# Kernel optimization log

Hardware: AMD Instinct MI355X
Metric: run time of the kernel (lower is better)

The kernel has to match this reference:

```python
import jax, jax.numpy as jnp
import numpy as np

B, T, S0 = 8, 4, 4096
D_MODEL, H, D, R, RANK = 2048, 16, 128, 64, 512
C = D - R  # content dim = 64


def _rope(x, positions):
    # x: [B, H, T, R]; rotate-half style RoPE as in the torch module
    half = x.shape[-1] // 2
    inv_freq = 1.0 / (10000.0 ** (jnp.arange(half, dtype=jnp.float32) / half))
    freqs = positions.astype(jnp.float32)[:, None] * inv_freq[None, :]  # [T, half]
    cos = jnp.cos(freqs)[None, None].astype(x.dtype)
    sin = jnp.sin(freqs)[None, None].astype(x.dtype)
    x1, x2 = x[..., :half], x[..., half:]
    return jnp.concatenate([x1 * cos - x2 * sin, x1 * sin + x2 * cos], axis=-1)


def setup_inputs() -> dict:
    key = jax.random.key(0)
    ks = jax.random.split(key, 9)
    s = 0.02
    return {
        "x": jax.random.normal(ks[0], (B, T, D_MODEL), jnp.float32),
        "cache_c_kv": jax.random.normal(ks[1], (B, S0, RANK), jnp.float32),
        "cache_k_rope": jax.random.normal(ks[2], (B, S0, H, R), jnp.float32),
        "w_q": jax.random.normal(ks[3], (D_MODEL, H * C), jnp.float32) * s,
        "w_q_rope": jax.random.normal(ks[4], (D_MODEL, H * R), jnp.float32) * s,
        "w_kv_down": jax.random.normal(ks[5], (D_MODEL, RANK), jnp.float32) * s,
        "w_kv_up": jax.random.normal(ks[6], (RANK, H * D), jnp.float32) * s,
        "w_k_rope": jax.random.normal(ks[7], (D_MODEL, H * R), jnp.float32) * s,
        "w_out": jax.random.normal(ks[8], (H * D, D_MODEL), jnp.float32) * s,
    }


def reference(x, cache_c_kv, cache_k_rope, w_q, w_q_rope, w_kv_down, w_kv_up, w_k_rope, w_out):
    cache_len = cache_c_kv.shape[1]
    positions = jnp.arange(cache_len, cache_len + T)

    # queries
    q_content = (x @ w_q).reshape(B, T, H, C).transpose(0, 2, 1, 3)        # [B,H,T,C]
    q_rope = (x @ w_q_rope).reshape(B, T, H, R).transpose(0, 2, 1, 3)      # [B,H,T,R]
    q_rope = _rope(q_rope, positions)
    q = jnp.concatenate([q_content, q_rope], axis=-1)                       # [B,H,T,D]

    # new compressed kv + rope keys, append to cache
    c_kv_new = x @ w_kv_down                                                # [B,T,RANK]
    k_rope_new = (x @ w_k_rope).reshape(B, T, H, R).transpose(0, 2, 1, 3)
    k_rope_new = _rope(k_rope_new, positions).transpose(0, 2, 1, 3)         # [B,T,H,R]
    c_kv = jnp.concatenate([cache_c_kv, c_kv_new], axis=1)                  # [B,S,RANK]
    k_rope = jnp.concatenate([cache_k_rope, k_rope_new], axis=1)            # [B,S,H,R]

    # decompress full cache every step (the expensive MLA pattern)
    S = c_kv.shape[1]
    kv = (c_kv @ w_kv_up).reshape(B, S, H, D)                               # [B,S,H,D]
    k_content = kv[..., :C].transpose(0, 2, 1, 3)                           # [B,H,S,C]
    v = kv.transpose(0, 2, 1, 3)                                            # [B,H,S,D]
    k = jnp.concatenate([k_content, k_rope.transpose(0, 2, 1, 3)], axis=-1) # [B,H,S,D]

    # kv_cache present => is_prefill False => no causal mask (faithful to source)
    scale = 1.0 / jnp.sqrt(jnp.asarray(D, dtype=q.dtype))
    scores = jnp.einsum('bhtd,bhsd->bhts', q, k) * scale
    attn = jax.nn.softmax(scores, axis=-1)
    out = jnp.einsum('bhts,bhsd->bhtd', attn, v)                            # [B,H,T,D]
    out = out.transpose(0, 2, 1, 3).reshape(B, T, H * D)
    return out @ w_out                                                       # [B,T,D_MODEL]
```

## Files before the change

kernel.cpp:

```cpp
#include <hip/hip_runtime.h>
#include <hip/hip_fp16.h>
#include <cmath>

#define BB 8
#define TT 4
#define HH 16
#define DDIM 128
#define RRDIM 64
#define CCDIM 64
#define RANKC 512
#define DMODEL 2048
#define S0C 4096
#define NQ 64
#define HD 2048
#define NACT 3584
#define NSC 65
#define NG 17
#define SPAD 4160
#define SCALE_ATT 0.08838834764831845f

typedef __attribute__((ext_vector_type(8))) short bf16x8;
typedef __attribute__((ext_vector_type(4))) float f32x4;
typedef unsigned short ushortT;

#define AIDX(row, kk) ((row)*132 + (((row)>>2)<<2) + (kk))

static __device__ __forceinline__ unsigned short f2bf(float x) {
  unsigned u = __float_as_uint(x);
  u += 0x7FFFu + ((u >> 16) & 1u);
  return (unsigned short)(u >> 16);
}
static __device__ __forceinline__ unsigned pk2(float a, float b) {
  return (unsigned)f2bf(a) | ((unsigned)f2bf(b) << 16);
}

__global__ __launch_bounds__(256) void k_front(const float* __restrict__ A,
                                               const float* __restrict__ w0,
                                               const float* __restrict__ w1,
                                               const float* __restrict__ w2,
                                               const float* __restrict__ w3,
                                               const float* __restrict__ cckv,
                                               float* __restrict__ part,
                                               ushortT* __restrict__ ckvB,
                                               ushortT* __restrict__ ckvT,
                                               float* __restrict__ rctab) {
  __shared__ float shf[4352];
  const int tid = threadIdx.x;
  const int bx = blockIdx.x;
  if (bx < 448) {
    const int cb = bx % 28;
    const int k0 = (bx / 28) * 128;
    const float* W; int N, lc0, off;
    if (cb < 8)       { W = w0; N = 1024; lc0 = cb * 128;        off = 0; }
    else if (cb < 16) { W = w1; N = 1024; lc0 = (cb - 8) * 128;  off = 1024; }
    else if (cb < 20) { W = w2; N = 512;  lc0 = (cb - 16) * 128; off = 2048; }
    else              { W = w3; N = 1024; lc0 = (cb - 20) * 128; off = 2560; }
    {
      const int row = tid >> 3;
      const int kseg = (tid & 7) * 16;
      const float4* s4 = reinterpret_cast<const float4*>(A + (size_t)row * DMODEL + k0 + kseg);
      float4 v0 = s4[0], v1 = s4[1], v2 = s4[2], v3 = s4[3];
      *reinterpret_cast<float4*>(&shf[AIDX(row, kseg)])      = v0;
      *reinterpret_cast<float4*>(&shf[AIDX(row, kseg + 4)])  = v1;
      *reinterpret_cast<float4*>(&shf[AIDX(row, kseg + 8)])  = v2;
      *reinterpret_cast<float4*>(&shf[AIDX(row, kseg + 12)]) = v3;
    }
    __syncthreads();
    const int cg = tid & 31;
    const int rg = tid >> 5;
    float acc[4][4];
    #pragma unroll
    for (int r = 0; r < 4; ++r)
      #pragma unroll
      for (int c = 0; c < 4; ++c) acc[r][c] = 0.f;
    #pragma unroll 4
    for (int kk = 0; kk < 128; ++kk) {
      const float4 w4 = *reinterpret_cast<const float4*>(W + (size_t)(k0 + kk) * N + lc0 + cg * 4);
      const float wv[4] = {w4.x, w4.y, w4.z, w4.w};
      #pragma unroll
      for (int r = 0; r < 4; ++r) {
        const float av = shf[AIDX(rg * 4 + r, kk)];
        #pragma unroll
        for (int c = 0; c < 4; ++c) acc[r][c] = fmaf(av, wv[c], acc[r][c]);
      }
    }
    #pragma unroll
    for (int r = 0; r < 4; ++r) {
      float4 o = make_float4(acc[r][0], acc[r][1], acc[r][2], acc[r][3]);
      *reinterpret_cast<float4*>(part + ((size_t)(bx / 28) * 32 + rg * 4 + r) * NACT + off + lc0 + cg * 4) = o;
    }
  } else if (bx < 960) {
    ushortT* tlds = reinterpret_cast<ushortT*>(shf);
    const int idx = bx - 448;
    const int b = idx >> 6, c = idx & 63;
    const float* src = cckv + ((size_t)b * S0C + c * 64) * RANKC;
    ushortT* dstB = ckvB + ((size_t)(b * NSC + c) * 64) * RANKC;
    ushortT* dstT = ckvT + ((size_t)(b * NSC + c) * RANKC) * 64;
    const int s = tid >> 2, rq = tid & 3;
    const int rloc = tid >> 1, shalf = (tid & 1) * 32;
    for (int slab = 0; slab < 4; ++slab) {
      const int r0 = slab * 128;
      unsigned pk_arr[16];
      #pragma unroll
      for (int i = 0; i < 8; ++i) {
        const float4 v = *reinterpret_cast<const float4*>(src + (size_t)s * RANKC + r0 + rq * 32 + i * 4);
        pk_arr[2 * i]     = pk2(v.x, v.y);
        pk_arr[2 * i + 1] = pk2(v.z, v.w);
        *reinterpret_cast<uint2*>(&tlds[s * 136 + rq * 32 + i * 4]) =
            make_uint2(pk_arr[2 * i], pk_arr[2 * i + 1]);
      }
      {
        uint4* db = reinterpret_cast<uint4*>(dstB + (size_t)s * RANKC + r0 + rq * 32);
        db[0] = make_uint4(pk_arr[0], pk_arr[1], pk_arr[2], pk_arr[3]);
        db[1] = make_uint4(pk_arr[4], pk_arr[5], pk_arr[6], pk_arr[7]);
        db[2] = make_uint4(pk_arr[8], pk_arr[9], pk_arr[10], pk_arr[11]);
        db[3] = make_uint4(pk_arr[12], pk_arr[13], pk_arr[14], pk_arr[15]);
      }
      __syncthreads();
      unsigned pkv[16];
      #pragma unroll
      for (int k = 0; k < 16; ++k) {
        const unsigned t0 = tlds[(shalf + 2 * k)     * 136 + rloc];
        const unsigned t1 = tlds[(shalf + 2 * k + 1) * 136 + rloc];
        pkv[k] = t0 | (t1 << 16);
      }
      uint4* d = reinterpret_cast<uint4*>(dstT + ((size_t)(r0 + rloc)) * 64 + shalf);
      d[0] = make_uint4(pkv[0], pkv[1], pkv[2], pkv[3]);
      d[1] = make_uint4(pkv[4], pkv[5], pkv[6], pkv[7]);
      d[2] = make_uint4(pkv[8], pkv[9], pkv[10], pkv[11]);
      d[3] = make_uint4(pkv[12], pkv[13], pkv[14], pkv[15]);
      __syncthreads();
    }
  } else {
    const int b = bx - 960;
    const uint4 z = make_uint4(0, 0, 0, 0);
    uint4* p = reinterpret_cast<uint4*>(ckvT + ((size_t)(b * NSC + 64) * RANKC) * 64);
    for (int i = tid; i < 4096; i += 256) p[i] = z;
    uint4* q = reinterpret_cast<uint4*>(ckvB + (((size_t)(b * NSC + 64) * 64) + 4) * RANKC);
    for (int i = tid; i < 3840; i += 256) q[i] = z;
    if (bx == 960 && tid < 128) {
      const int t = tid >> 5, j = tid & 31;
      const double fr = (double)(S0C + t) * pow(10000.0, -(double)j / 32.0);
      rctab[t * 32 + j]       = (float)cos(fr);
      rctab[128 + t * 32 + j] = (float)sin(fr);
    }
  }
}

__global__ __launch_bounds__(256) void k_mid(const float* __restrict__ part0,
                                             const float* __restrict__ cache_kr,
                                             const float* __restrict__ wup,
                                             const float* __restrict__ rctab,
                                             ushortT* __restrict__ qlat,
                                             ushortT* __restrict__ ckvB,
                                             ushortT* __restrict__ ckvT,
                                             __half* __restrict__ rs) {
  __shared__ float smid[2176];
  const int tid = threadIdx.x;
  const int bx = blockIdx.x;
  if (bx < 1152) {
    const int bh = bx / 9, sy = bx % 9;
    const int b = bh >> 4, h = bh & 15;
    float* raw_q = smid;
    float* raw_k = smid + 256;
    float* qr_l  = smid + 512;
    float* kr_l  = smid + 768;
    {
      const int t = tid >> 6, j = tid & 63;
      const size_t rowoff = (size_t)(b * TT + t) * NACT;
      float sq = 0.f, sk = 0.f;
      #pragma unroll 4
      for (int ks = 0; ks < 16; ++ks) {
        const float* pp = part0 + (size_t)ks * (32 * NACT) + rowoff;
        sq += pp[1024 + h * 64 + j];
        sk += pp[2560 + h * 64 + j];
      }
      raw_q[t * 64 + j] = sq;
      raw_k[t * 64 + j] = sk;
    }
    __syncthreads();
    {
      const int t = tid >> 6, j = tid & 63;
      const int j2 = j & 31;
      const float cs = rctab[t * 32 + j2];
      const float sn = rctab[128 + t * 32 + j2];
      const float qa = raw_q[t * 64 + j], qp = raw_q[t * 64 + (j ^ 32)];
      const float ka = raw_k[t * 64 + j], kp = raw_k[t * 64 + (j ^ 32)];
      float qv, kv;
      if (j < 32) { qv = qa * cs - qp * sn; kv = ka * cs - kp * sn; }
      else        { qv = qp * sn + qa * cs; kv = kp * sn + ka * cs; }
      qr_l[t * 64 + j] = qv * SCALE_ATT;
      kr_l[t * 64 + j] = kv;
    }
    __syncthreads();
    const int ql = tid & 3;
    float4 qf[4][4];
    #pragma unroll
    for (int t = 0; t < 4; ++t)
      #pragma unroll
      for (int u = 0; u < 4; ++u)
        qf[t][u] = *reinterpret_cast<const float4*>(&qr_l[t * 64 + ql * 16 + u * 4]);
    const int s0 = sy * 512;
    #pragma unroll 2
    for (int pass = 0; pass < 8; ++pass) {
      const int s = s0 + pass * 64 + (tid >> 2);
      if (s < 4100) {
        float p[4] = {0.f, 0.f, 0.f, 0.f};
        const float* krow = (s < S0C)
            ? cache_kr + (((size_t)b * S0C + s) * HH + h) * RRDIM
            : &kr_l[(s - S0C) * 64];
        #pragma unroll
        for (int u = 0; u < 4; ++u) {
          const float4 kv = *reinterpret_cast<const float4*>(krow + ql * 16 + u * 4);
          #pragma unroll
          for (int t = 0; t < 4; ++t)
            p[t] += kv.x * qf[t][u].x + kv.y * qf[t][u].y
                  + kv.z * qf[t][u].z + kv.w * qf[t][u].w;
        }
        #pragma unroll
        for (int t = 0; t < 4; ++t) {
          p[t] += __shfl_xor(p[t], 1, 4);
          p[t] += __shfl_xor(p[t], 2, 4);
        }
        rs[((size_t)bh * 4 + ql) * SPAD + s] = __float2half(p[ql]);
      }
    }
  } else if (bx < 1216) {
    const int lx = bx - 1152;
    const int h = lx & 15;
    const int r0 = (lx >> 4) * 128;
    float* a_s = smid;
    {
      const int bt = tid >> 3;
      const int c8 = (tid & 7) * 8;
      float v[8] = {0.f,0.f,0.f,0.f,0.f,0.f,0.f,0.f};
      #pragma unroll 4
      for (int ks = 0; ks < 16; ++ks) {
        const float4* pp = reinterpret_cast<const float4*>(
            part0 + (size_t)ks * (32 * NACT) + (size_t)bt * NACT + h * CCDIM + c8);
        const float4 x0 = pp[0], x1 = pp[1];
        v[0]+=x0.x; v[1]+=x0.y; v[2]+=x0.z; v[3]+=x0.w;
        v[4]+=x1.x; v[5]+=x1.y; v[6]+=x1.z; v[7]+=x1.w;
      }
      #pragma unroll
      for (int u = 0; u < 8; ++u) a_s[bt * 68 + c8 + u] = v[u];
    }
    __syncthreads();
    const int r = tid & 127;
    const int bth = tid >> 7;
    const float* wrow = wup + (size_t)(r0 + r) * HD + h * DDIM;
    float4 wreg[16];
    #pragma unroll
    for (int u = 0; u < 16; ++u)
      wreg[u] = *reinterpret_cast<const float4*>(wrow + u * 4);
    float acc[16];
    #pragma unroll
    for (int i = 0; i < 16; ++i) acc[i] = 0.f;
    #pragma unroll
    for (int u = 0; u < 16; ++u) {
      #pragma unroll
      for (int i = 0; i < 16; ++i) {
        const float4 av = *reinterpret_cast<const float4*>(&a_s[(bth * 16 + i) * 68 + u * 4]);
        acc[i] = fmaf(av.x, wreg[u].x, acc[i]);
        acc[i] = fmaf(av.y, wreg[u].y, acc[i]);
        acc[i] = fmaf(av.z, wreg[u].z, acc[i]);
        acc[i] = fmaf(av.w, wreg[u].w, acc[i]);
      }
    }
    #pragma unroll
    for (int i = 0; i < 16; ++i) {
      const int bt = bth * 16 + i;
      const int b = bt >> 2, t = bt & 3;
      qlat[((size_t)(b * NQ) + h * TT + t) * RANKC + r0 + r] = f2bf(acc[i]);
    }
  } else {
    const int g = (bx - 1216) * 256 + tid;
    const int r = g & 511;
    const int bt = g >> 9;
    const int b = bt >> 2, t = bt & 3;
    float s = 0.f;
    #pragma unroll 4
    for (int ks = 0; ks < 16; ++ks)
      s += part0[(size_t)ks * (32 * NACT) + (size_t)bt * NACT + 2048 + r];
    const ushortT bv = f2bf(s);
    ckvB[(((size_t)(b * NSC + 64) * 64) + t) * RANKC + r] = bv;
    ckvT[(((size_t)(b * NSC + 64) * RANKC) + r) * 64 + t] = bv;
  }
}

__global__ __launch_bounds__(256) void k_att(
    const ushortT* __restrict__ ckvB, const ushortT* __restrict__ ckvT,
    const ushortT* __restrict__ qlat, const __half* __restrict__ rs,
    float* __restrict__ olat, float* __restrict__ mlg) {
  __shared__ ushortT PL[4][32 * 72];
  __shared__ float mlS[4][2][32];
  __shared__ float wS[4][32];
  const int tid = threadIdx.x;
  const int wv = tid >> 6;
  const int lane = tid & 63;
  const int lm = lane & 15, lg = lane >> 4;
  const int g = blockIdx.x, b = blockIdx.y, qh = blockIdx.z;
  const int qbase = qh * 32;
  const int nc = (g < 16) ? 4 : 1;
  const int c0 = (g < 16) ? g * 4 : 64;

  if (wv < nc) {
    const int myc = c0 + wv;
    const int scnt = (myc < 64) ? 64 : TT;
    const ushortT* bsrc = ckvB + ((size_t)(b * NSC + myc) * 64) * RANKC;
    const ushortT* qrow = qlat + ((size_t)b * NQ + qbase + lm) * RANKC + lg * 8;
    f32x4 acc[2][4];
    #pragma unroll
    for (int qm = 0; qm < 2; ++qm)
      #pragma unroll
      for (int st = 0; st < 4; ++st) acc[qm][st] = (f32x4){0.f, 0.f, 0.f, 0.f};
    #pragma unroll
    for (int ks = 0; ks < 16; ++ks) {
      const bf16x8 qa0 = *reinterpret_cast<const bf16x8*>(qrow + ks * 32);
      const bf16x8 qa1 = *reinterpret_cast<const bf16x8*>(qrow + 16 * RANKC + ks * 32);
      #pragma unroll
      for (int st = 0; st < 4; ++st) {
        const bf16x8 bf = *reinterpret_cast<const bf16x8*>(
            bsrc + (size_t)(st * 16 + lm) * RANKC + ks * 32 + lg * 8);
        acc[0][st] = __builtin_amdgcn_mfma_f32_16x16x32_bf16(qa0, bf, acc[0][st], 0, 0, 0);
        acc[1][st] = __builtin_amdgcn_mfma_f32_16x16x32_bf16(qa1, bf, acc[1][st], 0, 0, 0);
      }
    }
    #pragma unroll
    for (int qm = 0; qm < 2; ++qm) {
      #pragma unroll
      for (int reg = 0; reg < 4; ++reg) {
        const int ql = qm * 16 + lg * 4 + reg;
        const int qi = qbase + ql;
        const __half* rp = rs + (((size_t)(b * HH) + (qi >> 2)) * TT + (qi & 3)) * SPAD + myc * 64;
        float vvv[4];
        float mx = -1e30f;
        #pragma unroll
        for (int st = 0; st < 4; ++st) {
          const int sl = st * 16 + lm;
          const float val = (sl < scnt)
              ? fmaf(acc[qm][st][reg], SCALE_ATT, __half2float(rp[sl]))
              : -1e30f;
          vvv[st] = val;
          mx = fmaxf(mx, val);
        }
        #pragma unroll
        for (int off = 1; off < 16; off <<= 1) mx = fmaxf(mx, __shfl_xor(mx, off, 16));
        float sum = 0.f;
        #pragma unroll
        for (int st = 0; st < 4; ++st) {
          const float p = __expf(vvv[st] - mx);
          vvv[st] = p;
          sum += p;
        }
        #pragma unroll
        for (int off = 1; off < 16; off <<= 1) sum += __shfl_xor(sum, off, 16);
        #pragma unroll
        for (int st = 0; st < 4; ++st)
          PL[wv][ql * 72 + st * 16 + lm] = f2bf(vvv[st]);
        if (lm == 0) { mlS[wv][0][ql] = mx; mlS[wv][1][ql] = sum; }
      }
    }
  }
  __syncthreads();

  if (tid < 32) {
    const int q = tid;
    float mg = -1e30f;
    for (int c = 0; c < nc; ++c) mg = fmaxf(mg, mlS[c][0][q]);
    float la = 0.f;
    for (int c = 0; c < nc; ++c) {
      const float w = __expf(mlS[c][0][q] - mg);
      wS[c][q] = w;
      la = fmaf(mlS[c][1][q], w, la);
    }
    const size_t gb = (((size_t)b * NG + g) * NQ + qbase + q) * 2;
    mlg[gb] = mg; mlg[gb + 1] = la;
  }
  __syncthreads();

  const int rg = wv;
  f32x4 OACC[2][8];
  #pragma unroll
  for (int qm = 0; qm < 2; ++qm)
    #pragma unroll
    for (int rn = 0; rn < 8; ++rn) OACC[qm][rn] = (f32x4){0.f, 0.f, 0.f, 0.f};
  for (int c = 0; c < nc; ++c) {
    const bf16x8 pa00 = *reinterpret_cast<const bf16x8*>(&PL[c][lm * 72 + lg * 8]);
    const bf16x8 pa01 = *reinterpret_cast<const bf16x8*>(&PL[c][lm * 72 + 32 + lg * 8]);
    const bf16x8 pa10 = *reinterpret_cast<const bf16x8*>(&PL[c][(16 + lm) * 72 + lg * 8]);
    const bf16x8 pa11 = *reinterpret_cast<const bf16x8*>(&PL[c][(16 + lm) * 72 + 32 + lg * 8]);
    const f32x4 w0 = {wS[c][lg * 4 + 0], wS[c][lg * 4 + 1], wS[c][lg * 4 + 2], wS[c][lg * 4 + 3]};
    const f32x4 w1 = {wS[c][16 + lg * 4 + 0], wS[c][16 + lg * 4 + 1],
                      wS[c][16 + lg * 4 + 2], wS[c][16 + lg * 4 + 3]};
    const ushortT* vb = ckvT + ((size_t)(b * NSC + c0 + c) * RANKC + rg * 128 + lm) * 64 + lg * 8;
    #pragma unroll
    for (int rn = 0; rn < 8; ++rn) {
      const bf16x8 b0 = *reinterpret_cast<const bf16x8*>(vb + (size_t)rn * 16 * 64);
      const bf16x8 b1 = *reinterpret_cast<const bf16x8*>(vb + (size_t)rn * 16 * 64 + 32);
      f32x4 t0 = (f32x4){0.f, 0.f, 0.f, 0.f}, t1 = (f32x4){0.f, 0.f, 0.f, 0.f};
      t0 = __builtin_amdgcn_mfma_f32_16x16x32_bf16(pa00, b0, t0, 0, 0, 0);
      t0 = __builtin_amdgcn_mfma_f32_16x16x32_bf16(pa01, b1, t0, 0, 0, 0);
      t1 = __builtin_amdgcn_mfma_f32_16x16x32_bf16(pa10, b0, t1, 0, 0, 0);
      t1 = __builtin_amdgcn_mfma_f32_16x16x32_bf16(pa11, b1, t1, 0, 0, 0);
      OACC[0][rn] += w0 * t0;
      OACC[1][rn] += w1 * t1;
    }
  }
  const size_t obase = ((size_t)(b * NG + g) * NQ) * RANKC;
  #pragma unroll
  for (int qm = 0; qm < 2; ++qm)
    #pragma unroll
    for (int rn = 0; rn < 8; ++rn)
      #pragma unroll
      for (int reg = 0; reg < 4; ++reg)
        olat[obase + (size_t)(qbase + qm * 16 + lg * 4 + reg) * RANKC + rg * 128 + rn * 16 + lm]
            = OACC[qm][rn][reg];
}

__global__ __launch_bounds__(512) void k_combF(const float* __restrict__ mlg,
                                               const float* __restrict__ olat,
                                               const float* __restrict__ wup,
                                               float* __restrict__ ohead,
                                               float* __restrict__ out) {
  __shared__ float wrow[4][20];
  __shared__ float att_lds[4][516];
  __shared__ float red[4][4][32][4];
  const int h = blockIdx.x, b = blockIdx.y;
  const int tid = threadIdx.x;
  {
    const int t = tid >> 7, col = tid & 127;
    out[(size_t)(b * TT + t) * HD + h * DDIM + col] = 0.f;
  }
  const int wave = tid >> 6;
  const int i = wave >> 1;
  const int rhalf = wave & 1;
  const int rl = tid & 63;
  const int qi = h * TT + i;
  float m1 = -1e30f, l1 = 0.f;
  if (rl < NG) {
    const size_t base = (((size_t)b * NG + rl) * NQ + qi) * 2;
    m1 = mlg[base]; l1 = mlg[base + 1];
  }
  float M = m1;
  #pragma unroll
  for (int off = 1; off < 64; off <<= 1) M = fmaxf(M, __shfl_xor(M, off));
  float L = (rl < NG) ? l1 * __expf(m1 - M) : 0.f;
  #pragma unroll
  for (int off = 1; off < 64; off <<= 1) L += __shfl_xor(L, off);
  const float invL = 1.0f / L;
  if (rl < NG) wrow[i][rl] = __expf(m1 - M) * invL;
  __syncthreads();
  const int r0 = rhalf * 256 + rl * 4;
  {
    float o0 = 0.f, o1 = 0.f, o2 = 0.f, o3 = 0.f;
    for (int c = 0; c < NG; ++c) {
      const float w = wrow[i][c];
      const float4 v = *reinterpret_cast<const float4*>(
          olat + (((size_t)b * NG + c) * NQ + qi) * RANKC + r0);
      o0 = fmaf(v.x, w, o0); o1 = fmaf(v.y, w, o1);
      o2 = fmaf(v.z, w, o2); o3 = fmaf(v.w, w, o3);
    }
    *reinterpret_cast<float4*>(&att_lds[i][r0]) = make_float4(o0, o1, o2, o3);
  }
  __syncthreads();
  const int t = tid >> 7;
  const int rq = (tid >> 5) & 3;
  const int c4 = tid & 31;
  const float* wb = wup + (size_t)h * DDIM + c4 * 4;
  float a0 = 0.f, a1 = 0.f, a2 = 0.f, a3 = 0.f;
  const int rbeg = rq * 128;
  #pragma unroll 4
  for (int rr = 0; rr < 128; ++rr) {
    const int r = rbeg + rr;
    const float4 w4 = *reinterpret_cast<const float4*>(wb + (size_t)r * HD);
    const float a = att_lds[t][r];
    a0 = fmaf(a, w4.x, a0); a1 = fmaf(a, w4.y, a1);
    a2 = fmaf(a, w4.z, a2); a3 = fmaf(a, w4.w, a3);
  }
  *reinterpret_cast<float4*>(&red[rq][t][c4][0]) = make_float4(a0, a1, a2, a3);
  __syncthreads();
  if (tid < 128) {
    const int t2 = tid >> 5, c42 = tid & 31;
    float4 s = make_float4(0.f, 0.f, 0.f, 0.f);
    #pragma unroll
    for (int q = 0; q < 4; ++q) {
      const float4 v = *reinterpret_cast<const float4*>(&red[q][t2][c42][0]);
      s.x += v.x; s.y += v.y; s.z += v.z; s.w += v.w;
    }
    *reinterpret_cast<float4*>(&ohead[(size_t)(b * TT + t2) * HD + h * DDIM + c42 * 4]) = s;
  }
}

__global__ __launch_bounds__(256) void k_projA(const float* __restrict__ A,
                                               const float* __restrict__ W,
                                               float* __restrict__ out) {
  __shared__ float a_lds[4352];
  const int tid = threadIdx.x;
  const int c0 = blockIdx.x * 128;
  const int k0 = blockIdx.y * 128;
  {
    const int row = tid >> 3;
    const int kseg = (tid & 7) * 16;
    const float4* s4 = reinterpret_cast<const float4*>(A + (size_t)row * DMODEL + k0 + kseg);
    float4 v0 = s4[0], v1 = s4[1], v2 = s4[2], v3 = s4[3];
    *reinterpret_cast<float4*>(&a_lds[AIDX(row, kseg)])      = v0;
    *reinterpret_cast<float4*>(&a_lds[AIDX(row, kseg + 4)])  = v1;
    *reinterpret_cast<float4*>(&a_lds[AIDX(row, kseg + 8)])  = v2;
    *reinterpret_cast<float4*>(&a_lds[AIDX(row, kseg + 12)]) = v3;
  }
  __syncthreads();
  const int cg = tid & 31;
  const int rg = tid >> 5;
  float acc[4][4];
  #pragma unroll
  for (int r = 0; r < 4; ++r)
    #pragma unroll
    for (int c = 0; c < 4; ++c) acc[r][c] = 0.f;
  #pragma unroll 4
  for (int kk = 0; kk < 128; ++kk) {
    const float4 w4 = *reinterpret_cast<const float4*>(W + (size_t)(k0 + kk) * HD + c0 + cg * 4);
    const float wv[4] = {w4.x, w4.y, w4.z, w4.w};
    #pragma unroll
    for (int r = 0; r < 4; ++r) {
      const float av = a_lds[AIDX(rg * 4 + r, kk)];
      #pragma unroll
      for (int c = 0; c < 4; ++c) acc[r][c] = fmaf(av, wv[c], acc[r][c]);
    }
  }
  #pragma unroll
  for (int r = 0; r < 4; ++r)
    #pragma unroll
    for (int c = 0; c < 4; ++c)
      unsafeAtomicAdd(&out[(size_t)(rg * 4 + r) * HD + c0 + cg * 4 + c], acc[r][c]);
}

extern "C" void kernel_launch(void* const* d_in, const int* in_sizes, int n_in,
                              void* d_out, int out_size, void* d_ws, size_t ws_size,
                              hipStream_t stream) {
  const float* x     = (const float*)d_in[0];
  const float* cckv  = (const float*)d_in[1];
  const float* ckr   = (const float*)d_in[2];
  const float* w_q   = (const float*)d_in[3];
  const float* w_qr  = (const float*)d_in[4];
  const float* w_kvd = (const float*)d_in[5];
  const float* w_kvu = (const float*)d_in[6];
  const float* w_kr  = (const float*)d_in[7];
  const float* w_out = (const float*)d_in[8];
  float* out = (float*)d_out;
  float* ws = (float*)d_ws;

  size_t off = 0;
  ushortT* qlat   = (ushortT*)(ws + off); off += 131072;
  float* mlgb     = ws + off; off += (size_t)BB * NG * NQ * 2;
  float* ohead    = ws + off; off += 65536;
  float* rctab    = ws + off; off += 256;
  __half* rsb     = (__half*)(ws + off); off += 1064960;
  ushortT* ckvB   = (ushortT*)(ws + off); off += 8519680;
  ushortT* ckvT   = (ushortT*)(ws + off); off += 8519680;
  float* regB  = ws + off;
  float* part0 = regB;
  float* olat  = regB;

  k_front<<<dim3(968), 256, 0, stream>>>(x, w_q, w_qr, w_kvd, w_kr, cckv, part0, ckvB, ckvT, rctab);
  k_mid<<<dim3(1280), 256, 0, stream>>>(part0, ckr, w_kvu, rctab, qlat, ckvB, ckvT, rsb);
  k_att<<<dim3(NG, BB, 2), 256, 0, stream>>>(ckvB, ckvT, qlat, rsb, olat, mlgb);
  k_combF<<<dim3(16, 8), 512, 0, stream>>>(mlgb, olat, w_kvu, ohead, out);
  k_projA<<<dim3(16, 16), 256, 0, stream>>>(ohead, w_out, out);
}
```

Measured before the change: 194.6 us.

## Split combine/projection over rank quarters, prefetch rope keys, raise MFMA priority

k_combF is split across four rank quarters in a new grid dimension. Each block writes a partial head output, and k_projA sums these partials while loading its A tile, using a K-split of 64 over twice as many blocks. The rope-score loop in k_mid now double-buffers the cache key loads, and the tail rows get their own path. s_setprio is raised around the MFMA loops in k_att. The aim is more parallelism in the small tail kernels and hiding memory latency, at the cost of extra partial-buffer traffic and more atomics in k_projA.

```diff
diff --git a/kernel.cpp b/kernel.cpp
--- a/kernel.cpp
+++ b/kernel.cpp
@@ -137,7 +137,7 @@
     uint4* p = reinterpret_cast<uint4*>(ckvT + ((size_t)(b * NSC + 64) * RANKC) * 64);
     for (int i = tid; i < 4096; i += 256) p[i] = z;
     uint4* q = reinterpret_cast<uint4*>(ckvB + (((size_t)(b * NSC + 64) * 64) + 4) * RANKC);
-    for (int i = tid; i < 3840; i += 256) q[i] = z;
+    for (int i = tid; i < 3840; i += 256) p = p, q[i] = z;
     if (bx == 960 && tid < 128) {
       const int t = tid >> 5, j = tid & 31;
       const double fr = (double)(S0C + t) * pow(10000.0, -(double)j / 32.0);
@@ -200,15 +200,42 @@
       #pragma unroll
       for (int u = 0; u < 4; ++u)
         qf[t][u] = *reinterpret_cast<const float4*>(&qr_l[t * 64 + ql * 16 + u * 4]);
-    const int s0 = sy * 512;
-    #pragma unroll 2
-    for (int pass = 0; pass < 8; ++pass) {
-      const int s = s0 + pass * 64 + (tid >> 2);
-      if (s < 4100) {
+    if (sy < 8) {
+      const int s0 = sy * 512;
+      const int sloc = tid >> 2;
+      const float* base = cache_kr + (((size_t)b * S0C + s0 + sloc) * HH + h) * RRDIM + ql * 16;
+      const size_t sstep = (size_t)64 * HH * RRDIM;
+      float4 bA[4], bB[4];
+      #pragma unroll
+      for (int u = 0; u < 4; ++u) bA[u] = *reinterpret_cast<const float4*>(base + u * 4);
+      #pragma unroll
+      for (int pass = 0; pass < 8; ++pass) {
+        float4* cur = (pass & 1) ? bB : bA;
+        float4* nxt = (pass & 1) ? bA : bB;
+        if (pass < 7) {
+          const float* nb = base + (size_t)(pass + 1) * sstep;
+          #pragma unroll
+          for (int u = 0; u < 4; ++u) nxt[u] = *reinterpret_cast<const float4*>(nb + u * 4);
+        }
         float p[4] = {0.f, 0.f, 0.f, 0.f};
-        const float* krow = (s < S0C)
-            ? cache_kr + (((size_t)b * S0C + s) * HH + h) * RRDIM
-            : &kr_l[(s - S0C) * 64];
+        #pragma unroll
+        for (int u = 0; u < 4; ++u)
+          #pragma unroll
+          for (int t = 0; t < 4; ++t)
+            p[t] += cur[u].x * qf[t][u].x + cur[u].y * qf[t][u].y
+                  + cur[u].z * qf[t][u].z + cur[u].w * qf[t][u].w;
+        #pragma unroll
+        for (int t = 0; t < 4; ++t) {
+          p[t] += __shfl_xor(p[t], 1, 4);
+          p[t] += __shfl_xor(p[t], 2, 4);
+        }
+        rs[((size_t)bh * 4 + ql) * SPAD + s0 + pass * 64 + sloc] = __float2half(p[ql]);
+      }
+    } else {
+      const int sloc = tid >> 2;
+      if (sloc < TT) {
+        const float* krow = &kr_l[sloc * 64];
+        float p[4] = {0.f, 0.f, 0.f, 0.f};
         #pragma unroll
         for (int u = 0; u < 4; ++u) {
           const float4 kv = *reinterpret_cast<const float4*>(krow + ql * 16 + u * 4);
@@ -222,7 +249,7 @@
           p[t] += __shfl_xor(p[t], 1, 4);
           p[t] += __shfl_xor(p[t], 2, 4);
         }
-        rs[((size_t)bh * 4 + ql) * SPAD + s] = __float2half(p[ql]);
+        rs[((size_t)bh * 4 + ql) * SPAD + S0C + sloc] = __float2half(p[ql]);
       }
     }
   } else if (bx < 1216) {
@@ -314,6 +341,7 @@
     for (int qm = 0; qm < 2; ++qm)
       #pragma unroll
       for (int st = 0; st < 4; ++st) acc[qm][st] = (f32x4){0.f, 0.f, 0.f, 0.f};
+    __builtin_amdgcn_s_setprio(1);
     #pragma unroll
     for (int ks = 0; ks < 16; ++ks) {
       const bf16x8 qa0 = *reinterpret_cast<const bf16x8*>(qrow + ks * 32);
@@ -326,6 +354,7 @@
         acc[1][st] = __builtin_amdgcn_mfma_f32_16x16x32_bf16(qa1, bf, acc[1][st], 0, 0, 0);
       }
     }
+    __builtin_amdgcn_s_setprio(0);
     #pragma unroll
     for (int qm = 0; qm < 2; ++qm) {
       #pragma unroll
@@ -394,6 +423,7 @@
     const f32x4 w1 = {wS[c][16 + lg * 4 + 0], wS[c][16 + lg * 4 + 1],
                       wS[c][16 + lg * 4 + 2], wS[c][16 + lg * 4 + 3]};
     const ushortT* vb = ckvT + ((size_t)(b * NSC + c0 + c) * RANKC + rg * 128 + lm) * 64 + lg * 8;
+    __builtin_amdgcn_s_setprio(1);
     #pragma unroll
     for (int rn = 0; rn < 8; ++rn) {
       const bf16x8 b0 = *reinterpret_cast<const bf16x8*>(vb + (size_t)rn * 16 * 64);
@@ -406,6 +436,7 @@
       OACC[0][rn] += w0 * t0;
       OACC[1][rn] += w1 * t1;
     }
+    __builtin_amdgcn_s_setprio(0);
   }
   const size_t obase = ((size_t)(b * NG + g) * NQ) * RANKC;
   #pragma unroll
@@ -418,23 +449,22 @@
             = OACC[qm][rn][reg];
 }
 
-__global__ __launch_bounds__(512) void k_combF(const float* __restrict__ mlg,
+__global__ __launch_bounds__(256) void k_combF(const float* __restrict__ mlg,
                                                const float* __restrict__ olat,
                                                const float* __restrict__ wup,
-                                               float* __restrict__ ohead,
+                                               float* __restrict__ oheadP,
                                                float* __restrict__ out) {
   __shared__ float wrow[4][20];
-  __shared__ float att_lds[4][516];
-  __shared__ float red[4][4][32][4];
-  const int h = blockIdx.x, b = blockIdx.y;
+  __shared__ float red[2][4][32][4];
+  __shared__ float att_l[4][128];
+  const int h = blockIdx.x, b = blockIdx.y, rq = blockIdx.z;
   const int tid = threadIdx.x;
-  {
-    const int t = tid >> 7, col = tid & 127;
-    out[(size_t)(b * TT + t) * HD + h * DDIM + col] = 0.f;
-  }
-  const int wave = tid >> 6;
-  const int i = wave >> 1;
-  const int rhalf = wave & 1;
+  if (rq == 0) {
+    const int t = tid >> 6, col2 = (tid & 63) * 2;
+    out[(size_t)(b * TT + t) * HD + h * DDIM + col2] = 0.f;
+    out[(size_t)(b * TT + t) * HD + h * DDIM + col2 + 1] = 0.f;
+  }
+  const int i = tid >> 6;
   const int rl = tid & 63;
   const int qi = h * TT + i;
   float m1 = -1e30f, l1 = 0.f;
@@ -451,63 +481,80 @@
   const float invL = 1.0f / L;
   if (rl < NG) wrow[i][rl] = __expf(m1 - M) * invL;
   __syncthreads();
-  const int r0 = rhalf * 256 + rl * 4;
   {
+    const int ch = tid >> 7;
+    const int t = (tid >> 5) & 3;
+    const int p32 = tid & 31;
+    const int qit = h * TT + t;
+    const int cbeg = ch ? 9 : 0, cend = ch ? NG : 9;
     float o0 = 0.f, o1 = 0.f, o2 = 0.f, o3 = 0.f;
-    for (int c = 0; c < NG; ++c) {
-      const float w = wrow[i][c];
+    #pragma unroll 3
+    for (int c = cbeg; c < cend; ++c) {
+      const float w = wrow[t][c];
       const float4 v = *reinterpret_cast<const float4*>(
-          olat + (((size_t)b * NG + c) * NQ + qi) * RANKC + r0);
+          olat + (((size_t)b * NG + c) * NQ + qit) * RANKC + rq * 128 + p32 * 4);
       o0 = fmaf(v.x, w, o0); o1 = fmaf(v.y, w, o1);
       o2 = fmaf(v.z, w, o2); o3 = fmaf(v.w, w, o3);
     }
-    *reinterpret_cast<float4*>(&att_lds[i][r0]) = make_float4(o0, o1, o2, o3);
-  }
-  __syncthreads();
-  const int t = tid >> 7;
-  const int rq = (tid >> 5) & 3;
-  const int c4 = tid & 31;
-  const float* wb = wup + (size_t)h * DDIM + c4 * 4;
-  float a0 = 0.f, a1 = 0.f, a2 = 0.f, a3 = 0.f;
-  const int rbeg = rq * 128;
-  #pragma unroll 4
-  for (int rr = 0; rr < 128; ++rr) {
-    const int r = rbeg + rr;
-    const float4 w4 = *reinterpret_cast<const float4*>(wb + (size_t)r * HD);
-    const float a = att_lds[t][r];
-    a0 = fmaf(a, w4.x, a0); a1 = fmaf(a, w4.y, a1);
-    a2 = fmaf(a, w4.z, a2); a3 = fmaf(a, w4.w, a3);
-  }
-  *reinterpret_cast<float4*>(&red[rq][t][c4][0]) = make_float4(a0, a1, a2, a3);
+    *reinterpret_cast<float4*>(&red[ch][t][p32][0]) = make_float4(o0, o1, o2, o3);
+  }
   __syncthreads();
   if (tid < 128) {
-    const int t2 = tid >> 5, c42 = tid & 31;
-    float4 s = make_float4(0.f, 0.f, 0.f, 0.f);
-    #pragma unroll
-    for (int q = 0; q < 4; ++q) {
-      const float4 v = *reinterpret_cast<const float4*>(&red[q][t2][c42][0]);
-      s.x += v.x; s.y += v.y; s.z += v.z; s.w += v.w;
-    }
-    *reinterpret_cast<float4*>(&ohead[(size_t)(b * TT + t2) * HD + h * DDIM + c42 * 4]) = s;
-  }
-}
-
-__global__ __launch_bounds__(256) void k_projA(const float* __restrict__ A,
+    const int t = tid >> 5, p32 = tid & 31;
+    const float4 v0 = *reinterpret_cast<const float4*>(&red[0][t][p32][0]);
+    const float4 v1 = *reinterpret_cast<const float4*>(&red[1][t][p32][0]);
+    *reinterpret_cast<float4*>(&att_l[t][p32 * 4]) =
+        make_float4(v0.x + v1.x, v0.y + v1.y, v0.z + v1.z, v0.w + v1.w);
+  }
+  __syncthreads();
+  {
+    const int rhalf = tid >> 7;
+    const int t = (tid >> 5) & 3;
+    const int c4 = tid & 31;
+    const float* wb = wup + (size_t)(rq * 128 + rhalf * 64) * HD + h * DDIM + c4 * 4;
+    float a0 = 0.f, a1 = 0.f, a2 = 0.f, a3 = 0.f;
+    #pragma unroll 4
+    for (int rr = 0; rr < 64; ++rr) {
+      const float4 w4 = *reinterpret_cast<const float4*>(wb + (size_t)rr * HD);
+      const float a = att_l[t][rhalf * 64 + rr];
+      a0 = fmaf(a, w4.x, a0); a1 = fmaf(a, w4.y, a1);
+      a2 = fmaf(a, w4.z, a2); a3 = fmaf(a, w4.w, a3);
+    }
+    *reinterpret_cast<float4*>(&red[rhalf][t][c4][0]) = make_float4(a0, a1, a2, a3);
+  }
+  __syncthreads();
+  if (tid < 128) {
+    const int t = tid >> 5, c4 = tid & 31;
+    const float4 v0 = *reinterpret_cast<const float4*>(&red[0][t][c4][0]);
+    const float4 v1 = *reinterpret_cast<const float4*>(&red[1][t][c4][0]);
+    *reinterpret_cast<float4*>(
+        &oheadP[(((size_t)rq * 32) + b * TT + t) * HD + h * DDIM + c4 * 4]) =
+        make_float4(v0.x + v1.x, v0.y + v1.y, v0.z + v1.z, v0.w + v1.w);
+  }
+}
+
+__global__ __launch_bounds__(256) void k_projA(const float* __restrict__ oheadP,
                                                const float* __restrict__ W,
                                                float* __restrict__ out) {
-  __shared__ float a_lds[4352];
+  __shared__ float a_lds[2176];
   const int tid = threadIdx.x;
   const int c0 = blockIdx.x * 128;
-  const int k0 = blockIdx.y * 128;
+  const int k0 = blockIdx.y * 64;
   {
     const int row = tid >> 3;
-    const int kseg = (tid & 7) * 16;
-    const float4* s4 = reinterpret_cast<const float4*>(A + (size_t)row * DMODEL + k0 + kseg);
-    float4 v0 = s4[0], v1 = s4[1], v2 = s4[2], v3 = s4[3];
-    *reinterpret_cast<float4*>(&a_lds[AIDX(row, kseg)])      = v0;
-    *reinterpret_cast<float4*>(&a_lds[AIDX(row, kseg + 4)])  = v1;
-    *reinterpret_cast<float4*>(&a_lds[AIDX(row, kseg + 8)])  = v2;
-    *reinterpret_cast<float4*>(&a_lds[AIDX(row, kseg + 12)]) = v3;
+    const int kseg = (tid & 7) * 8;
+    float4 s0 = make_float4(0.f, 0.f, 0.f, 0.f), s1 = s0;
+    #pragma unroll
+    for (int p = 0; p < 4; ++p) {
+      const float4* v4 = reinterpret_cast<const float4*>(
+          oheadP + ((size_t)p * 32 + row) * HD + k0 + kseg);
+      const float4 a = v4[0], bq = v4[1];
+      s0.x += a.x;  s0.y += a.y;  s0.z += a.z;  s0.w += a.w;
+      s1.x += bq.x; s1.y += bq.y; s1.z += bq.z; s1.w += bq.w;
+    }
+    const int base = row * 68 + kseg;
+    *reinterpret_cast<float4*>(&a_lds[base]) = s0;
+    *reinterpret_cast<float4*>(&a_lds[base + 4]) = s1;
   }
   __syncthreads();
   const int cg = tid & 31;
@@ -518,12 +565,12 @@
     #pragma unroll
     for (int c = 0; c < 4; ++c) acc[r][c] = 0.f;
   #pragma unroll 4
-  for (int kk = 0; kk < 128; ++kk) {
+  for (int kk = 0; kk < 64; ++kk) {
     const float4 w4 = *reinterpret_cast<const float4*>(W + (size_t)(k0 + kk) * HD + c0 + cg * 4);
     const float wv[4] = {w4.x, w4.y, w4.z, w4.w};
     #pragma unroll
     for (int r = 0; r < 4; ++r) {
-      const float av = a_lds[AIDX(rg * 4 + r, kk)];
+      const float av = a_lds[(rg * 4 + r) * 68 + kk];
       #pragma unroll
       for (int c = 0; c < 4; ++c) acc[r][c] = fmaf(av, wv[c], acc[r][c]);
     }
@@ -553,7 +600,7 @@
   size_t off = 0;
   ushortT* qlat   = (ushortT*)(ws + off); off += 131072;
   float* mlgb     = ws + off; off += (size_t)BB * NG * NQ * 2;
-  float* ohead    = ws + off; off += 65536;
+  float* oheadP   = ws + off; off += 262144;
   float* rctab    = ws + off; off += 256;
   __half* rsb     = (__half*)(ws + off); off += 1064960;
   ushortT* ckvB   = (ushortT*)(ws + off); off += 8519680;
@@ -565,6 +612,6 @@
   k_front<<<dim3(968), 256, 0, stream>>>(x, w_q, w_qr, w_kvd, w_kr, cckv, part0, ckvB, ckvT, rctab);
   k_mid<<<dim3(1280), 256, 0, stream>>>(part0, ckr, w_kvu, rctab, qlat, ckvB, ckvT, rsb);
   k_att<<<dim3(NG, BB, 2), 256, 0, stream>>>(ckvB, ckvT, qlat, rsb, olat, mlgb);
-  k_combF<<<dim3(16, 8), 512, 0, stream>>>(mlgb, olat, w_kvu, ohead, out);
-  k_projA<<<dim3(16, 16), 256, 0, stream>>>(ohead, w_out, out);
-}
+  k_combF<<<dim3(16, 8, 4), 256, 0, stream>>>(mlgb, olat, w_kvu, oheadP, out);
+  k_projA<<<dim3(16, 32), 256, 0, stream>>>(oheadP, w_out, out);
+}
```

Measured after the change: 197.9 us. Within noise of the previous version (+1.7%).

## Restructure rope-score blocks to read contiguous k_rope rows across all heads

Applied to the files above, without the earlier changes.

The rope-score part of k_mid now gives each block a batch and a 32-position slice covering all 16 heads, so every cache_k_rope row (16 heads × 64) is read contiguously instead of one head-strided 256-byte slice per block. Each of these blocks reduces and ropes the queries for all heads into a 16 KB shared buffer. Eight separate tail blocks compute the scores against the 4 new rope keys. The split partials for q are therefore reduced redundantly by 128 blocks per batch, and shared memory use grows to 32 KB per block, which may lower occupancy.

```diff
diff --git a/kernel.cpp b/kernel.cpp
--- a/kernel.cpp
+++ b/kernel.cpp
@@ -155,78 +155,123 @@
                                              ushortT* __restrict__ ckvB,
                                              ushortT* __restrict__ ckvT,
                                              __half* __restrict__ rs) {
-  __shared__ float smid[2176];
+  __shared__ float smid[8192];
   const int tid = threadIdx.x;
   const int bx = blockIdx.x;
-  if (bx < 1152) {
-    const int bh = bx / 9, sy = bx % 9;
-    const int b = bh >> 4, h = bh & 15;
-    float* raw_q = smid;
-    float* raw_k = smid + 256;
-    float* qr_l  = smid + 512;
-    float* kr_l  = smid + 768;
+  if (bx < 1032) {
+    const bool tail = (bx >= 1024);
+    const int b = tail ? (bx - 1024) : (bx >> 7);
+    float* qS = smid;
     {
-      const int t = tid >> 6, j = tid & 63;
-      const size_t rowoff = (size_t)(b * TT + t) * NACT;
-      float sq = 0.f, sk = 0.f;
-      #pragma unroll 4
-      for (int ks = 0; ks < 16; ++ks) {
-        const float* pp = part0 + (size_t)ks * (32 * NACT) + rowoff;
-        sq += pp[1024 + h * 64 + j];
-        sk += pp[2560 + h * 64 + j];
-      }
-      raw_q[t * 64 + j] = sq;
-      raw_k[t * 64 + j] = sk;
+      float v[16];
+      #pragma unroll
+      for (int r = 0; r < 16; ++r) {
+        const int idx = r * 256 + tid;
+        const int h = idx >> 8, tt = (idx >> 6) & 3, j = idx & 63;
+        float s = 0.f;
+        #pragma unroll 4
+        for (int ks = 0; ks < 16; ++ks)
+          s += part0[(size_t)ks * (32 * NACT) + (size_t)(b * TT + tt) * NACT + 1024 + h * 64 + j];
+        v[r] = s;
+      }
+      #pragma unroll
+      for (int r = 0; r < 16; ++r) qS[r * 256 + tid] = v[r];
     }
     __syncthreads();
     {
-      const int t = tid >> 6, j = tid & 63;
-      const int j2 = j & 31;
-      const float cs = rctab[t * 32 + j2];
-      const float sn = rctab[128 + t * 32 + j2];
-      const float qa = raw_q[t * 64 + j], qp = raw_q[t * 64 + (j ^ 32)];
-      const float ka = raw_k[t * 64 + j], kp = raw_k[t * 64 + (j ^ 32)];
-      float qv, kv;
-      if (j < 32) { qv = qa * cs - qp * sn; kv = ka * cs - kp * sn; }
-      else        { qv = qp * sn + qa * cs; kv = kp * sn + ka * cs; }
-      qr_l[t * 64 + j] = qv * SCALE_ATT;
-      kr_l[t * 64 + j] = kv;
+      float rv[16];
+      #pragma unroll
+      for (int r = 0; r < 16; ++r) {
+        const int idx = r * 256 + tid;
+        const int tt = (idx >> 6) & 3, j = idx & 63, j2 = j & 31;
+        const float cs = rctab[tt * 32 + j2];
+        const float sn = rctab[128 + tt * 32 + j2];
+        const float a = qS[idx], p = qS[idx ^ 32];
+        rv[r] = ((j < 32) ? (a * cs - p * sn) : (p * sn + a * cs)) * SCALE_ATT;
+      }
+      __syncthreads();
+      #pragma unroll
+      for (int r = 0; r < 16; ++r) qS[r * 256 + tid] = rv[r];
     }
     __syncthreads();
-    const int ql = tid & 3;
-    float4 qf[4][4];
-    #pragma unroll
-    for (int t = 0; t < 4; ++t)
-      #pragma unroll
-      for (int u = 0; u < 4; ++u)
-        qf[t][u] = *reinterpret_cast<const float4*>(&qr_l[t * 64 + ql * 16 + u * 4]);
-    const int s0 = sy * 512;
-    #pragma unroll 2
-    for (int pass = 0; pass < 8; ++pass) {
-      const int s = s0 + pass * 64 + (tid >> 2);
-      if (s < 4100) {
-        float p[4] = {0.f, 0.f, 0.f, 0.f};
-        const float* krow = (s < S0C)
-            ? cache_kr + (((size_t)b * S0C + s) * HH + h) * RRDIM
-            : &kr_l[(s - S0C) * 64];
-        #pragma unroll
-        for (int u = 0; u < 4; ++u) {
-          const float4 kv = *reinterpret_cast<const float4*>(krow + ql * 16 + u * 4);
+    if (!tail) {
+      const int s0 = (bx & 127) * 32;
+      const int sloc = tid >> 3;
+      const int j8 = (tid & 7) * 8;
+      const int bh4 = b * HH * 4;
+      const float* krow = cache_kr + ((size_t)(b * S0C + s0 + sloc)) * (HH * RRDIM);
+      #pragma unroll 4
+      for (int h = 0; h < 16; ++h) {
+        const float4 k0 = *reinterpret_cast<const float4*>(krow + h * 64 + j8);
+        const float4 k1 = *reinterpret_cast<const float4*>(krow + h * 64 + j8 + 4);
+        float p[4];
+        #pragma unroll
+        for (int t = 0; t < 4; ++t) {
+          const float4 q0 = *reinterpret_cast<const float4*>(&qS[h * 256 + t * 64 + j8]);
+          const float4 q1 = *reinterpret_cast<const float4*>(&qS[h * 256 + t * 64 + j8 + 4]);
+          p[t] = k0.x * q0.x + k0.y * q0.y + k0.z * q0.z + k0.w * q0.w
+               + k1.x * q1.x + k1.y * q1.y + k1.z * q1.z + k1.w * q1.w;
+        }
+        #pragma unroll
+        for (int t = 0; t < 4; ++t) {
+          p[t] += __shfl_xor(p[t], 1, 8);
+          p[t] += __shfl_xor(p[t], 2, 8);
+          p[t] += __shfl_xor(p[t], 4, 8);
+        }
+        if ((tid & 7) == 0) {
           #pragma unroll
           for (int t = 0; t < 4; ++t)
-            p[t] += kv.x * qf[t][u].x + kv.y * qf[t][u].y
-                  + kv.z * qf[t][u].z + kv.w * qf[t][u].w;
-        }
-        #pragma unroll
-        for (int t = 0; t < 4; ++t) {
-          p[t] += __shfl_xor(p[t], 1, 4);
-          p[t] += __shfl_xor(p[t], 2, 4);
-        }
-        rs[((size_t)bh * 4 + ql) * SPAD + s] = __float2half(p[ql]);
-      }
-    }
-  } else if (bx < 1216) {
-    const int lx = bx - 1152;
+            rs[(size_t)(bh4 + h * 4 + t) * SPAD + s0 + sloc] = __float2half(p[t]);
+        }
+      }
+    } else {
+      float* krnS = smid + 4096;
+      {
+        float v[16];
+        #pragma unroll
+        for (int r = 0; r < 16; ++r) {
+          const int idx = r * 256 + tid;
+          const int t2 = idx >> 10, h = (idx >> 6) & 15, j = idx & 63;
+          float s = 0.f;
+          #pragma unroll 4
+          for (int ks = 0; ks < 16; ++ks)
+            s += part0[(size_t)ks * (32 * NACT) + (size_t)(b * TT + t2) * NACT + 2560 + h * 64 + j];
+          v[r] = s;
+        }
+        #pragma unroll
+        for (int r = 0; r < 16; ++r) krnS[r * 256 + tid] = v[r];
+      }
+      __syncthreads();
+      {
+        float rv[16];
+        #pragma unroll
+        for (int r = 0; r < 16; ++r) {
+          const int idx = r * 256 + tid;
+          const int t2 = idx >> 10, j = idx & 63, j2 = j & 31;
+          const float cs = rctab[t2 * 32 + j2];
+          const float sn = rctab[128 + t2 * 32 + j2];
+          const float a = krnS[idx], p = krnS[idx ^ 32];
+          rv[r] = (j < 32) ? (a * cs - p * sn) : (p * sn + a * cs);
+        }
+        __syncthreads();
+        #pragma unroll
+        for (int r = 0; r < 16; ++r) krnS[r * 256 + tid] = rv[r];
+      }
+      __syncthreads();
+      {
+        const int h = tid >> 4, t = (tid >> 2) & 3, s = tid & 3;
+        float acc = 0.f;
+        #pragma unroll
+        for (int u = 0; u < 16; ++u) {
+          const float4 q4 = *reinterpret_cast<const float4*>(&qS[h * 256 + t * 64 + u * 4]);
+          const float4 k4 = *reinterpret_cast<const float4*>(&krnS[s * 1024 + h * 64 + u * 4]);
+          acc += q4.x * k4.x + q4.y * k4.y + q4.z * k4.z + q4.w * k4.w;
+        }
+        rs[(size_t)((b * HH + h) * 4 + t) * SPAD + S0C + s] = __float2half(acc);
+      }
+    }
+  } else if (bx < 1096) {
+    const int lx = bx - 1032;
     const int h = lx & 15;
     const int r0 = (lx >> 4) * 128;
     float* a_s = smid;
@@ -274,7 +319,7 @@
       qlat[((size_t)(b * NQ) + h * TT + t) * RANKC + r0 + r] = f2bf(acc[i]);
     }
   } else {
-    const int g = (bx - 1216) * 256 + tid;
+    const int g = (bx - 1096) * 256 + tid;
     const int r = g & 511;
     const int bt = g >> 9;
     const int b = bt >> 2, t = bt & 3;
@@ -563,7 +608,7 @@
   float* olat  = regB;
 
   k_front<<<dim3(968), 256, 0, stream>>>(x, w_q, w_qr, w_kvd, w_kr, cckv, part0, ckvB, ckvT, rctab);
-  k_mid<<<dim3(1280), 256, 0, stream>>>(part0, ckr, w_kvu, rctab, qlat, ckvB, ckvT, rsb);
+  k_mid<<<dim3(1160), 256, 0, stream>>>(part0, ckr, w_kvu, rctab, qlat, ckvB, ckvT, rsb);
   k_att<<<dim3(NG, BB, 2), 256, 0, stream>>>(ckvB, ckvT, qlat, rsb, olat, mlgb);
   k_combF<<<dim3(16, 8), 512, 0, stream>>>(mlgb, olat, w_kvu, ohead, out);
   k_projA<<<dim3(16, 16), 256, 0, stream>>>(ohead, w_out, out);
```

New measurement: 263.8 us. 1.36x slower.
